# Performance work log

Hardware: AMD Instinct MI355X
Metric: run time of the kernel (lower is better)

Reference implementation:

```python
import jax, jax.numpy as jnp
import numpy as np

N = 50000      # num nodes (genes)
E = 800000     # num edges (TF->Target)
IN = 128       # in_channels
HID = 16       # hidden_channels per head
HEADS = 4
OUT = 32       # out_channels
NEG_SLOPE = 0.2  # PyG GATConv leaky_relu slope
EPS = 1e-16


def setup_inputs() -> dict:
    key = jax.random.key(0)
    ks = jax.random.split(key, 11)
    x = jax.random.normal(ks[0], (N, IN), dtype=jnp.float32)
    edge_index = jax.random.randint(ks[1], (2, E), 0, N, dtype=jnp.int32)
    # layer 1: heads=HEADS, concat=True
    W1 = jax.random.normal(ks[2], (IN, HEADS * HID), dtype=jnp.float32) * (1.0 / np.sqrt(IN))
    a_src1 = jax.random.normal(ks[3], (HEADS, HID), dtype=jnp.float32) * 0.1
    a_dst1 = jax.random.normal(ks[4], (HEADS, HID), dtype=jnp.float32) * 0.1
    b1 = jnp.zeros((HEADS * HID,), dtype=jnp.float32)
    # layer 2: heads=1, concat=False
    W2 = jax.random.normal(ks[5], (HEADS * HID, OUT), dtype=jnp.float32) * (1.0 / np.sqrt(HEADS * HID))
    a_src2 = jax.random.normal(ks[6], (1, OUT), dtype=jnp.float32) * 0.1
    a_dst2 = jax.random.normal(ks[7], (1, OUT), dtype=jnp.float32) * 0.1
    b2 = jnp.zeros((OUT,), dtype=jnp.float32)
    return dict(x=x, edge_index=edge_index, W1=W1, a_src1=a_src1, a_dst1=a_dst1, b1=b1,
                W2=W2, a_src2=a_src2, a_dst2=a_dst2, b2=b2)


def gat_layer(x, edge_index, W, a_src, a_dst, b, concat):
    """PyG GATConv (no self-loops, eval mode): gather -> edge attention -> segment softmax -> scatter."""
    n = x.shape[0]
    heads, ch = a_src.shape
    h = (x @ W).reshape(n, heads, ch)                      # [N, H, C]
    alpha_s = jnp.einsum('nhc,hc->nh', h, a_src)           # [N, H]
    alpha_d = jnp.einsum('nhc,hc->nh', h, a_dst)           # [N, H]
    src, dst = edge_index[0], edge_index[1]
    e = jax.nn.leaky_relu(alpha_s[src] + alpha_d[dst], negative_slope=NEG_SLOPE)  # [E, H]
    # numerically stable softmax over incoming edges of each dst node
    m = jax.ops.segment_max(e, dst, num_segments=n)        # [N, H]
    e = jnp.exp(e - m[dst])
    denom = jax.ops.segment_sum(e, dst, num_segments=n)    # [N, H]
    alpha = e / (denom[dst] + EPS)                         # [E, H]
    msg = h[src] * alpha[:, :, None]                       # [E, H, C]
    out = jax.ops.segment_sum(msg, dst, num_segments=n)    # [N, H, C]
    if concat:
        out = out.reshape(n, heads * ch)
    else:
        out = out.mean(axis=1)
    return out + b


def reference(x, edge_index, W1, a_src1, a_dst1, b1, W2, a_src2, a_dst2, b2):
    h = gat_layer(x, edge_index, W1, a_src1, a_dst1, b1, concat=True)   # [N, HEADS*HID]
    h = jax.nn.elu(h)
    out = gat_layer(h, edge_index, W2, a_src2, a_dst2, b2, concat=False)  # [N, OUT]
    return out
```

## Files before the change

kernel.cpp:

```cpp
#include <hip/hip_runtime.h>
#include <math.h>

#define NN 50000
#define NE 800000
#define INCH 128
#define HID1 16
#define H1 4
#define C1 64
#define C2 32
#define NEG 0.2f
#define EPSF 1e-16f
#define CAP 128
#define BSH 7
#define NBKT 391
#define CAPB 3072
#define EPB 2048
#define NPB1 391

static __device__ __forceinline__ float lrelu(float v){ return v > 0.f ? v : NEG * v; }


__global__ __launch_bounds__(256) void k_part1(const int* __restrict__ ei, int* bcnt,
                                               int2* __restrict__ pairs){
    __shared__ int hist[512];
    __shared__ int scn[512];
    __shared__ int spos[512];
    __shared__ int gbase[NBKT];
    __shared__ int2 stg[EPB];
    int t = threadIdx.x;
    hist[t] = 0; hist[t + 256] = 0;
    __syncthreads();

    int e0 = blockIdx.x * EPB;
    int tot = NE - e0; if (tot > EPB) tot = EPB;
    int srcv[8], dstv[8], rnk[8], bkt[8];
    #pragma unroll
    for (int k = 0; k < 8; ++k){
        int idx = k * 256 + t;
        if (idx < tot){
            int e = e0 + idx;
            srcv[k] = ei[e];
            dstv[k] = ei[NE + e];
            bkt[k] = dstv[k] >> BSH;
            rnk[k] = atomicAdd(&hist[bkt[k]], 1);
        } else bkt[k] = -1;
    }
    __syncthreads();

    int* sA = hist; int* sB = scn;
    for (int off = 1; off < 512; off <<= 1){
        int v0 = sA[t]       + ((t       >= off) ? sA[t - off]       : 0);
        int v1 = sA[t + 256] + ((t + 256 >= off) ? sA[t + 256 - off] : 0);
        __syncthreads();
        sB[t] = v0; sB[t + 256] = v1;
        __syncthreads();
        int* tmp = sA; sA = sB; sB = tmp;
    }
    for (int b = t; b < NBKT; b += 256){
        int incl = sA[b];
        int excl = (b > 0) ? sA[b - 1] : 0;
        spos[b] = excl;
        int cnt = incl - excl;
        gbase[b] = (cnt > 0) ? atomicAdd(&bcnt[b], cnt) : 0;
    }
    __syncthreads();

    #pragma unroll
    for (int k = 0; k < 8; ++k)
        if (bkt[k] >= 0){
            int2 pr; pr.x = srcv[k]; pr.y = dstv[k];
            stg[spos[bkt[k]] + rnk[k]] = pr;
        }
    __syncthreads();

    for (int i = t; i < tot; i += 256){
        int2 pr = stg[i];
        int b = pr.y >> BSH;
        pairs[(size_t)b * CAPB + gbase[b] + (i - spos[b])] = pr;
    }
}

__global__ __launch_bounds__(256) void k_part2(const int2* __restrict__ pairs,
                                               const int* __restrict__ bcnt,
                                               int* __restrict__ rows, int* __restrict__ deg,
                                               int* __restrict__ srcs){
    __shared__ int2 stg[CAPB];
    __shared__ int hist[128], scn[128], cur[128];
    int b = blockIdx.x, t = threadIdx.x;
    int n0 = b << BSH;
    int cnt = bcnt[b];
    if (t < 128) hist[t] = 0;
    __syncthreads();
    const int2* psrc = pairs + (size_t)b * CAPB;
    for (int i = t; i < cnt; i += 256){
        int2 pr = psrc[i];
        stg[i] = pr;
        atomicAdd(&hist[pr.y - n0], 1);
    }
    __syncthreads();
    int v = (t < 128) ? hist[t] : 0;
    if (t < 128) scn[t] = v;
    __syncthreads();
    for (int off = 1; off < 128; off <<= 1){
        int add = (t < 128 && t >= off) ? scn[t - off] : 0;
        __syncthreads();
        if (t < 128) scn[t] += add;
        __syncthreads();
    }
    if (t < 128){
        int base = b * CAPB + (scn[t] - v);
        cur[t] = base;
        int n = n0 + t;
        if (n < NN){ rows[n] = base; deg[n] = v; }
    }
    __syncthreads();
    for (int i = t; i < cnt; i += 256){
        int2 pr = stg[i];
        int p = atomicAdd(&cur[pr.y - n0], 1);
        srcs[p] = pr.x;
    }
}


__global__ void k_gemm1(const float* __restrict__ x, const float* __restrict__ W,
                        const float* __restrict__ asrc, const float* __restrict__ adst,
                        float* __restrict__ h, float* __restrict__ as1, float* __restrict__ ad1){
    __shared__ float XT[INCH][68];
    __shared__ float WS[INCH * C1];
    __shared__ float ps[64][17];
    __shared__ float pd[64][17];

    int t = threadIdx.x;
    int nodeL = t >> 2;
    int kc = t & 3;
    int g = blockIdx.x * 64 + nodeL;
    int gc = min(g, NN - 1);
    const float4* xr = (const float4*)(x + (size_t)gc * INCH);
    #pragma unroll
    for (int i = 0; i < 8; ++i){
        int k = kc * 32 + i * 4;
        float4 v = xr[k >> 2];
        XT[k + 0][nodeL] = v.x;
        XT[k + 1][nodeL] = v.y;
        XT[k + 2][nodeL] = v.z;
        XT[k + 3][nodeL] = v.w;
    }
    const float4* W4 = (const float4*)W;
    float4* WS4 = (float4*)WS;
    #pragma unroll
    for (int i = 0; i < 8; ++i) WS4[i * 256 + t] = W4[i * 256 + t];
    __syncthreads();

    int tx = t & 15, ty = t >> 4;
    int c4 = tx * 4, n4 = ty * 4;
    float acc[4][4];
    #pragma unroll
    for (int a = 0; a < 4; ++a)
        #pragma unroll
        for (int b = 0; b < 4; ++b) acc[a][b] = 0.f;

    #pragma unroll 8
    for (int k = 0; k < INCH; ++k){
        float4 xa = *(const float4*)&XT[k][n4];
        float4 wb = *(const float4*)&WS[k * C1 + c4];
        const float xv[4] = {xa.x, xa.y, xa.z, xa.w};
        const float wv[4] = {wb.x, wb.y, wb.z, wb.w};
        #pragma unroll
        for (int a = 0; a < 4; ++a)
            #pragma unroll
            for (int b = 0; b < 4; ++b)
                acc[a][b] = fmaf(xv[a], wv[b], acc[a][b]);
    }

    int hd = tx >> 2;
    #pragma unroll
    for (int a = 0; a < 4; ++a){
        int n = blockIdx.x * 64 + n4 + a;
        if (n < NN){
            float4 o = {acc[a][0], acc[a][1], acc[a][2], acc[a][3]};
            *(float4*)&h[(size_t)n * C1 + c4] = o;
        }
        float sa = 0.f, da = 0.f;
        #pragma unroll
        for (int b = 0; b < 4; ++b){
            float wsv = asrc[hd * HID1 + (c4 & 15) + b];
            float wdv = adst[hd * HID1 + (c4 & 15) + b];
            sa = fmaf(acc[a][b], wsv, sa);
            da = fmaf(acc[a][b], wdv, da);
        }
        ps[n4 + a][tx] = sa;
        pd[n4 + a][tx] = da;
    }
    __syncthreads();
    int nd = t & 63, hh = t >> 6;
    int g2 = blockIdx.x * 64 + nd;
    if (g2 < NN){
        float sa = ps[nd][hh*4+0] + ps[nd][hh*4+1] + ps[nd][hh*4+2] + ps[nd][hh*4+3];
        float da = pd[nd][hh*4+0] + pd[nd][hh*4+1] + pd[nd][hh*4+2] + pd[nd][hh*4+3];
        as1[g2 * H1 + hh] = sa;
        ad1[g2 * H1 + hh] = da;
    }
}


__global__ void k_gemm2(const float* __restrict__ hp, const float* __restrict__ W2,
                        const float* __restrict__ asrc, const float* __restrict__ adst,
                        float* __restrict__ h2, float* __restrict__ as2, float* __restrict__ ad2){
    __shared__ float XT[C1][132];
    __shared__ float WS[C1 * C2];
    __shared__ float ps[128][9];
    __shared__ float pd[128][9];

    int t = threadIdx.x;
    int nodeL = t >> 1;
    int kc = t & 1;
    int g = blockIdx.x * 128 + nodeL;
    int gc = min(g, NN - 1);
    const float4* xr = (const float4*)(hp + (size_t)gc * C1);
    #pragma unroll
    for (int i = 0; i < 8; ++i){
        int k = kc * 32 + i * 4;
        float4 v = xr[k >> 2];
        XT[k + 0][nodeL] = v.x;
        XT[k + 1][nodeL] = v.y;
        XT[k + 2][nodeL] = v.z;
        XT[k + 3][nodeL] = v.w;
    }
    const float4* W4 = (const float4*)W2;
    float4* WS4 = (float4*)WS;
    #pragma unroll
    for (int i = 0; i < 2; ++i) WS4[i * 256 + t] = W4[i * 256 + t];
    __syncthreads();

    int tx = t & 7, ty = t >> 3;
    int c4 = tx * 4, n4 = ty * 4;
    float acc[4][4];
    #pragma unroll
    for (int a = 0; a < 4; ++a)
        #pragma unroll
        for (int b = 0; b < 4; ++b) acc[a][b] = 0.f;

    #pragma unroll 8
    for (int k = 0; k < C1; ++k){
        float4 xa = *(const float4*)&XT[k][n4];
        float4 wb = *(const float4*)&WS[k * C2 + c4];
        const float xv[4] = {xa.x, xa.y, xa.z, xa.w};
        const float wv[4] = {wb.x, wb.y, wb.z, wb.w};
        #pragma unroll
        for (int a = 0; a < 4; ++a)
            #pragma unroll
            for (int b = 0; b < 4; ++b)
                acc[a][b] = fmaf(xv[a], wv[b], acc[a][b]);
    }

    #pragma unroll
    for (int a = 0; a < 4; ++a){
        int n = blockIdx.x * 128 + n4 + a;
        if (n < NN){
            float4 o = {acc[a][0], acc[a][1], acc[a][2], acc[a][3]};
            *(float4*)&h2[(size_t)n * C2 + c4] = o;
        }
        float sa = 0.f, da = 0.f;
        #pragma unroll
        for (int b = 0; b < 4; ++b){
            sa = fmaf(acc[a][b], asrc[c4 + b], sa);
            da = fmaf(acc[a][b], adst[c4 + b], da);
        }
        ps[n4 + a][tx] = sa;
        pd[n4 + a][tx] = da;
    }
    __syncthreads();
    if (t < 128){
        int n = blockIdx.x * 128 + t;
        if (n < NN){
            float sa = 0.f, da = 0.f;
            #pragma unroll
            for (int i = 0; i < 8; ++i){ sa += ps[t][i]; da += pd[t][i]; }
            as2[n] = sa;
            ad2[n] = da;
        }
    }
}


__global__ __launch_bounds__(256) void k_agg1(
        const int* __restrict__ srcs, const int* __restrict__ rows,
        const int* __restrict__ deg, const float* __restrict__ h,
        const float* __restrict__ as, const float* __restrict__ ad,
        const float* __restrict__ b1, float* __restrict__ hp){
    __shared__ float vbuf[4][CAP * H1];
    __shared__ int   sbuf[4][CAP];
    __shared__ float minv[4][8];
    int wv = threadIdx.x >> 6;
    int lane = threadIdx.x & 63;
    int node = blockIdx.x * 4 + wv;
    int hd = lane >> 4, sub = lane & 15;
    int start = rows[node], dg = deg[node];
    float adv = ad[node * H1 + hd];
    bool fits = (dg <= CAP);

    float m = -1e30f, ssum = 0.f;
    for (int j = sub; j < dg; j += 16){
        int s = srcs[start + j];
        float v = lrelu(as[s * H1 + hd] + adv);
        if (fits){
            vbuf[wv][j * H1 + hd] = v;
            if (hd == 0) sbuf[wv][j] = s;
        }
        float nm = fmaxf(m, v);
        ssum = ssum * __expf(m - nm) + __expf(v - nm);
        m = nm;
    }
    #pragma unroll
    for (int off = 1; off < 16; off <<= 1){
        float om = __shfl_xor(m, off);
        float os = __shfl_xor(ssum, off);
        float nm = fmaxf(m, om);
        ssum = ssum * __expf(m - nm) + os * __expf(om - nm);
        m = nm;
    }
    float inv = 1.f / (ssum + EPSF);
    if (sub == 0){ minv[wv][hd] = m; minv[wv][4 + hd] = inv; }
    __syncthreads();

    if (fits){
        int tot = dg * H1;
        for (int it = lane; it < tot; it += 64){
            int th = it & 3;
            vbuf[wv][it] = __expf(vbuf[wv][it] - minv[wv][th]) * minv[wv][4 + th];
        }
    }
    __syncthreads();

    float acc0 = 0.f, acc1 = 0.f;
    const float* hL = h + lane;
    if (fits){
        int j = 0;
        for (; j + 3 < dg; j += 4){
            int s0 = sbuf[wv][j], s1 = sbuf[wv][j+1], s2 = sbuf[wv][j+2], s3 = sbuf[wv][j+3];
            float w0 = vbuf[wv][(j+0)*H1+hd], w1 = vbuf[wv][(j+1)*H1+hd];
            float w2 = vbuf[wv][(j+2)*H1+hd], w3 = vbuf[wv][(j+3)*H1+hd];
            float g0 = hL[(size_t)s0 * C1], g1 = hL[(size_t)s1 * C1];
            float g2 = hL[(size_t)s2 * C1], g3 = hL[(size_t)s3 * C1];
            acc0 = fmaf(g0, w0, acc0);
            acc1 = fmaf(g1, w1, acc1);
            acc0 = fmaf(g2, w2, acc0);
            acc1 = fmaf(g3, w3, acc1);
        }
        for (; j < dg; ++j)
            acc0 = fmaf(hL[(size_t)sbuf[wv][j] * C1], vbuf[wv][j*H1+hd], acc0);
    } else {
        for (int j = 0; j < dg; ++j){
            int s = srcs[start + j];
            float v = lrelu(as[s * H1 + hd] + adv);
            acc0 = fmaf(hL[(size_t)s * C1], __expf(v - m) * inv, acc0);
        }
    }
    float o = acc0 + acc1 + b1[lane];
    hp[(size_t)node * C1 + lane] = o > 0.f ? o : expm1f(o);
}

__global__ __launch_bounds__(256) void k_agg2(
        const int* __restrict__ srcs, const int* __restrict__ rows,
        const int* __restrict__ deg, const float* __restrict__ h2,
        const float* __restrict__ as, const float* __restrict__ ad,
        const float* __restrict__ b2, float* __restrict__ out){
    __shared__ float vbuf[8][CAP];
    __shared__ int   sbuf[8][CAP];
    int sl = threadIdx.x >> 5;
    int lane = threadIdx.x & 31;
    int node = blockIdx.x * 8 + sl;
    int start = rows[node], dg = deg[node];
    float adv = ad[node];
    bool fits = (dg <= CAP);

    float m = -1e30f, ssum = 0.f;
    for (int j = lane; j < dg; j += 32){
        int s = srcs[start + j];
        float v = lrelu(as[s] + adv);
        if (fits){ vbuf[sl][j] = v; sbuf[sl][j] = s; }
        float nm = fmaxf(m, v);
        ssum = ssum * __expf(m - nm) + __expf(v - nm);
        m = nm;
    }
    #pragma unroll
    for (int off = 1; off < 32; off <<= 1){
        float om = __shfl_xor(m, off);
        float os = __shfl_xor(ssum, off);
        float nm = fmaxf(m, om);
        ssum = ssum * __expf(m - nm) + os * __expf(om - nm);
        m = nm;
    }
    float inv = 1.f / (ssum + EPSF);
    if (fits)
        for (int j = lane; j < dg; j += 32)
            vbuf[sl][j] = __expf(vbuf[sl][j] - m) * inv;
    __syncthreads();

    float acc0 = 0.f, acc1 = 0.f;
    const float* hL = h2 + lane;
    if (fits){
        int j = 0;
        for (; j + 3 < dg; j += 4){
            int s0 = sbuf[sl][j], s1 = sbuf[sl][j+1], s2 = sbuf[sl][j+2], s3 = sbuf[sl][j+3];
            float w0 = vbuf[sl][j], w1 = vbuf[sl][j+1], w2 = vbuf[sl][j+2], w3 = vbuf[sl][j+3];
            float g0 = hL[(size_t)s0 * C2], g1 = hL[(size_t)s1 * C2];
            float g2 = hL[(size_t)s2 * C2], g3 = hL[(size_t)s3 * C2];
            acc0 = fmaf(g0, w0, acc0);
            acc1 = fmaf(g1, w1, acc1);
            acc0 = fmaf(g2, w2, acc0);
            acc1 = fmaf(g3, w3, acc1);
        }
        for (; j < dg; ++j)
            acc0 = fmaf(hL[(size_t)sbuf[sl][j] * C2], vbuf[sl][j], acc0);
    } else {
        for (int j = 0; j < dg; ++j){
            int s = srcs[start + j];
            acc0 = fmaf(hL[(size_t)s * C2], __expf(lrelu(as[s] + adv) - m) * inv, acc0);
        }
    }
    out[(size_t)node * C2 + lane] = acc0 + acc1 + b2[lane];
}

extern "C" void kernel_launch(void* const* d_in, const int* in_sizes, int n_in,
                              void* d_out, int out_size, void* d_ws, size_t ws_size,
                              hipStream_t stream) {
    const float* x    = (const float*)d_in[0];
    const int*   ei   = (const int*)  d_in[1];
    const float* W1   = (const float*)d_in[2];
    const float* as1w = (const float*)d_in[3];
    const float* ad1w = (const float*)d_in[4];
    const float* b1   = (const float*)d_in[5];
    const float* W2   = (const float*)d_in[6];
    const float* as2w = (const float*)d_in[7];
    const float* ad2w = (const float*)d_in[8];
    const float* b2   = (const float*)d_in[9];
    float* out = (float*)d_out;

    float* p = (float*)d_ws;
    float* h1   = p; p += (size_t)NN * C1;
    float* hp   = p; p += (size_t)NN * C1;
    float* as1  = p; p += (size_t)NN * H1;
    float* ad1  = p; p += (size_t)NN * H1;
    float* h2   = p; p += (size_t)NN * C2;
    float* as2  = p; p += NN;
    float* ad2  = p; p += NN;
    int* deg  = (int*)p; p += NN;
    int* rows = (int*)p; p += NN;
    int* bcnt = (int*)p; p += NBKT;
    int* srcs = (int*)p; p += (size_t)NBKT * CAPB;
    int2* pairs = (int2*)h1;

    dim3 B(256);
    hipMemsetAsync(bcnt, 0, NBKT * sizeof(int), stream);
    k_part1 <<<NPB1, B, 0, stream>>>(ei, bcnt, pairs);
    k_part2 <<<NBKT, B, 0, stream>>>(pairs, bcnt, rows, deg, srcs);
    k_gemm1 <<<(NN + 63) / 64, B, 0, stream>>>(x, W1, as1w, ad1w, h1, as1, ad1);
    k_agg1  <<<NN / 4, B, 0, stream>>>(srcs, rows, deg, h1, as1, ad1, b1, hp);
    k_gemm2 <<<(NN + 127) / 128, B, 0, stream>>>(hp, W2, as2w, ad2w, h2, as2, ad2);
    k_agg2  <<<NN / 8, B, 0, stream>>>(srcs, rows, deg, h2, as2, ad2, b2, out);
}
```

Before: 205.1 us.

## Fuse CSR build with GEMM1, fuse agg1 with GEMM2, drop softmax max pass

The CSR bucket build and the layer-1 GEMM now run as one launch, with blocks split by blockIdx, so both can overlap. Layer-1 aggregation is fused with the layer-2 GEMM and attention projection, so the hp intermediate is never written or read back. Both aggregation kernels drop the max-subtracted two-pass softmax in favour of a single pass that sums unnormalized exp weights and divides once at the end. That removes the shared-memory staging and a second pass over the edges, but exp can overflow if attention logits grow large.

```diff
diff --git a/kernel.cpp b/kernel.cpp
--- a/kernel.cpp
+++ b/kernel.cpp
@@ -10,12 +10,12 @@
 #define C2 32
 #define NEG 0.2f
 #define EPSF 1e-16f
-#define CAP 128
 #define BSH 7
 #define NBKT 391
 #define CAPB 3072
 #define EPB 2048
 #define NPB1 391
+#define GB1 782
 
 static __device__ __forceinline__ float lrelu(float v){ return v > 0.f ? v : NEG * v; }
 
@@ -80,346 +80,237 @@
     }
 }
 
-__global__ __launch_bounds__(256) void k_part2(const int2* __restrict__ pairs,
-                                               const int* __restrict__ bcnt,
-                                               int* __restrict__ rows, int* __restrict__ deg,
-                                               int* __restrict__ srcs){
-    __shared__ int2 stg[CAPB];
-    __shared__ int hist[128], scn[128], cur[128];
-    int b = blockIdx.x, t = threadIdx.x;
-    int n0 = b << BSH;
-    int cnt = bcnt[b];
-    if (t < 128) hist[t] = 0;
-    __syncthreads();
-    const int2* psrc = pairs + (size_t)b * CAPB;
-    for (int i = t; i < cnt; i += 256){
-        int2 pr = psrc[i];
-        stg[i] = pr;
-        atomicAdd(&hist[pr.y - n0], 1);
-    }
-    __syncthreads();
-    int v = (t < 128) ? hist[t] : 0;
-    if (t < 128) scn[t] = v;
-    __syncthreads();
-    for (int off = 1; off < 128; off <<= 1){
-        int add = (t < 128 && t >= off) ? scn[t - off] : 0;
-        __syncthreads();
-        if (t < 128) scn[t] += add;
-        __syncthreads();
-    }
-    if (t < 128){
-        int base = b * CAPB + (scn[t] - v);
-        cur[t] = base;
-        int n = n0 + t;
-        if (n < NN){ rows[n] = base; deg[n] = v; }
-    }
-    __syncthreads();
-    for (int i = t; i < cnt; i += 256){
-        int2 pr = stg[i];
-        int p = atomicAdd(&cur[pr.y - n0], 1);
-        srcs[p] = pr.x;
-    }
-}
-
-
-__global__ void k_gemm1(const float* __restrict__ x, const float* __restrict__ W,
-                        const float* __restrict__ asrc, const float* __restrict__ adst,
-                        float* __restrict__ h, float* __restrict__ as1, float* __restrict__ ad1){
-    __shared__ float XT[INCH][68];
-    __shared__ float WS[INCH * C1];
-    __shared__ float ps[64][17];
-    __shared__ float pd[64][17];
-
+
+__global__ __launch_bounds__(256) void k_build2(
+        const int2* __restrict__ pairs, const int* __restrict__ bcnt,
+        int* __restrict__ rows, int* __restrict__ deg, int* __restrict__ srcs,
+        const float* __restrict__ x, const float* __restrict__ W,
+        const float* __restrict__ asrc, const float* __restrict__ adst,
+        float* __restrict__ h, float* __restrict__ as1, float* __restrict__ ad1){
+    __shared__ __align__(16) char smem[76288];
     int t = threadIdx.x;
-    int nodeL = t >> 2;
-    int kc = t & 3;
-    int g = blockIdx.x * 64 + nodeL;
-    int gc = min(g, NN - 1);
-    const float4* xr = (const float4*)(x + (size_t)gc * INCH);
-    #pragma unroll
-    for (int i = 0; i < 8; ++i){
-        int k = kc * 32 + i * 4;
-        float4 v = xr[k >> 2];
-        XT[k + 0][nodeL] = v.x;
-        XT[k + 1][nodeL] = v.y;
-        XT[k + 2][nodeL] = v.z;
-        XT[k + 3][nodeL] = v.w;
-    }
-    const float4* W4 = (const float4*)W;
-    float4* WS4 = (float4*)WS;
-    #pragma unroll
-    for (int i = 0; i < 8; ++i) WS4[i * 256 + t] = W4[i * 256 + t];
-    __syncthreads();
-
-    int tx = t & 15, ty = t >> 4;
-    int c4 = tx * 4, n4 = ty * 4;
-    float acc[4][4];
-    #pragma unroll
-    for (int a = 0; a < 4; ++a)
+
+    if (blockIdx.x < NBKT){
+        int2* stg = (int2*)smem;
+        int* hist = (int*)(smem + 24576);
+        int* scn  = (int*)(smem + 25088);
+        int* cur  = (int*)(smem + 25600);
+        int b = blockIdx.x;
+        int n0 = b << BSH;
+        int cnt = bcnt[b];
+        if (t < 128) hist[t] = 0;
+        __syncthreads();
+        const int2* psrc = pairs + (size_t)b * CAPB;
+        for (int i = t; i < cnt; i += 256){
+            int2 pr = psrc[i];
+            stg[i] = pr;
+            atomicAdd(&hist[pr.y - n0], 1);
+        }
+        __syncthreads();
+        int v = (t < 128) ? hist[t] : 0;
+        if (t < 128) scn[t] = v;
+        __syncthreads();
+        for (int off = 1; off < 128; off <<= 1){
+            int add = (t < 128 && t >= off) ? scn[t - off] : 0;
+            __syncthreads();
+            if (t < 128) scn[t] += add;
+            __syncthreads();
+        }
+        if (t < 128){
+            int base = b * CAPB + (scn[t] - v);
+            cur[t] = base;
+            int n = n0 + t;
+            if (n < NN){ rows[n] = base; deg[n] = v; }
+        }
+        __syncthreads();
+        for (int i = t; i < cnt; i += 256){
+            int2 pr = stg[i];
+            int p = atomicAdd(&cur[pr.y - n0], 1);
+            srcs[p] = pr.x;
+        }
+    } else {
+        float (*XT)[68] = (float(*)[68])smem;
+        float* WS = (float*)(smem + 34816);
+        float (*ps)[17] = (float(*)[17])(smem + 67584);
+        float (*pd)[17] = (float(*)[17])(smem + 71936);
+        int bid = blockIdx.x - NBKT;
+
+        int nodeL = t >> 2;
+        int kc = t & 3;
+        int g = bid * 64 + nodeL;
+        int gc = min(g, NN - 1);
+        const float4* xr = (const float4*)(x + (size_t)gc * INCH);
         #pragma unroll
-        for (int b = 0; b < 4; ++b) acc[a][b] = 0.f;
-
-    #pragma unroll 8
-    for (int k = 0; k < INCH; ++k){
-        float4 xa = *(const float4*)&XT[k][n4];
-        float4 wb = *(const float4*)&WS[k * C1 + c4];
-        const float xv[4] = {xa.x, xa.y, xa.z, xa.w};
-        const float wv[4] = {wb.x, wb.y, wb.z, wb.w};
+        for (int i = 0; i < 8; ++i){
+            int k = kc * 32 + i * 4;
+            float4 v = xr[k >> 2];
+            XT[k + 0][nodeL] = v.x;
+            XT[k + 1][nodeL] = v.y;
+            XT[k + 2][nodeL] = v.z;
+            XT[k + 3][nodeL] = v.w;
+        }
+        const float4* W4 = (const float4*)W;
+        float4* WS4 = (float4*)WS;
+        #pragma unroll
+        for (int i = 0; i < 8; ++i) WS4[i * 256 + t] = W4[i * 256 + t];
+        __syncthreads();
+
+        int tx = t & 15, ty = t >> 4;
+        int c4 = tx * 4, n4 = ty * 4;
+        float acc[4][4];
         #pragma unroll
         for (int a = 0; a < 4; ++a)
             #pragma unroll
-            for (int b = 0; b < 4; ++b)
-                acc[a][b] = fmaf(xv[a], wv[b], acc[a][b]);
-    }
-
-    int hd = tx >> 2;
+            for (int b2 = 0; b2 < 4; ++b2) acc[a][b2] = 0.f;
+
+        #pragma unroll 8
+        for (int k = 0; k < INCH; ++k){
+            float4 xa = *(const float4*)&XT[k][n4];
+            float4 wb = *(const float4*)&WS[k * C1 + c4];
+            const float xv[4] = {xa.x, xa.y, xa.z, xa.w};
+            const float wv[4] = {wb.x, wb.y, wb.z, wb.w};
+            #pragma unroll
+            for (int a = 0; a < 4; ++a)
+                #pragma unroll
+                for (int b2 = 0; b2 < 4; ++b2)
+                    acc[a][b2] = fmaf(xv[a], wv[b2], acc[a][b2]);
+        }
+
+        int hd = tx >> 2;
+        #pragma unroll
+        for (int a = 0; a < 4; ++a){
+            int n = bid * 64 + n4 + a;
+            if (n < NN){
+                float4 o = {acc[a][0], acc[a][1], acc[a][2], acc[a][3]};
+                *(float4*)&h[(size_t)n * C1 + c4] = o;
+            }
+            float sa = 0.f, da = 0.f;
+            #pragma unroll
+            for (int b2 = 0; b2 < 4; ++b2){
+                sa = fmaf(acc[a][b2], asrc[hd * HID1 + (c4 & 15) + b2], sa);
+                da = fmaf(acc[a][b2], adst[hd * HID1 + (c4 & 15) + b2], da);
+            }
+            ps[n4 + a][tx] = sa;
+            pd[n4 + a][tx] = da;
+        }
+        __syncthreads();
+        int nd = t & 63, hh = t >> 6;
+        int g2 = bid * 64 + nd;
+        if (g2 < NN){
+            float sa = ps[nd][hh*4+0] + ps[nd][hh*4+1] + ps[nd][hh*4+2] + ps[nd][hh*4+3];
+            float da = pd[nd][hh*4+0] + pd[nd][hh*4+1] + pd[nd][hh*4+2] + pd[nd][hh*4+3];
+            as1[g2 * H1 + hh] = sa;
+            ad1[g2 * H1 + hh] = da;
+        }
+    }
+}
+
+
+__global__ __launch_bounds__(256) void k_aggA(
+        const int* __restrict__ srcs, const int* __restrict__ rows,
+        const int* __restrict__ deg, const float* __restrict__ h1,
+        const float* __restrict__ as, const float* __restrict__ ad,
+        const float* __restrict__ b1, const float* __restrict__ W2,
+        const float* __restrict__ a2s, const float* __restrict__ a2d,
+        float* __restrict__ h2, float* __restrict__ as2, float* __restrict__ ad2){
+    __shared__ float hpT[16][65];
+    __shared__ float WS[C1 * C2];
+    int t = threadIdx.x;
+    {
+        const float4* W4 = (const float4*)W2;
+        float4* WS4 = (float4*)WS;
+        WS4[t] = W4[t];
+        WS4[256 + t] = W4[256 + t];
+    }
+    int w = t >> 6, lane = t & 63, hd = lane >> 4;
+    float bv = b1[lane];
     #pragma unroll
-    for (int a = 0; a < 4; ++a){
-        int n = blockIdx.x * 64 + n4 + a;
-        if (n < NN){
-            float4 o = {acc[a][0], acc[a][1], acc[a][2], acc[a][3]};
-            *(float4*)&h[(size_t)n * C1 + c4] = o;
-        }
-        float sa = 0.f, da = 0.f;
-        #pragma unroll
-        for (int b = 0; b < 4; ++b){
-            float wsv = asrc[hd * HID1 + (c4 & 15) + b];
-            float wdv = adst[hd * HID1 + (c4 & 15) + b];
-            sa = fmaf(acc[a][b], wsv, sa);
-            da = fmaf(acc[a][b], wdv, da);
-        }
-        ps[n4 + a][tx] = sa;
-        pd[n4 + a][tx] = da;
-    }
-    __syncthreads();
-    int nd = t & 63, hh = t >> 6;
-    int g2 = blockIdx.x * 64 + nd;
-    if (g2 < NN){
-        float sa = ps[nd][hh*4+0] + ps[nd][hh*4+1] + ps[nd][hh*4+2] + ps[nd][hh*4+3];
-        float da = pd[nd][hh*4+0] + pd[nd][hh*4+1] + pd[nd][hh*4+2] + pd[nd][hh*4+3];
-        as1[g2 * H1 + hh] = sa;
-        ad1[g2 * H1 + hh] = da;
-    }
-}
-
-
-__global__ void k_gemm2(const float* __restrict__ hp, const float* __restrict__ W2,
-                        const float* __restrict__ asrc, const float* __restrict__ adst,
-                        float* __restrict__ h2, float* __restrict__ as2, float* __restrict__ ad2){
-    __shared__ float XT[C1][132];
-    __shared__ float WS[C1 * C2];
-    __shared__ float ps[128][9];
-    __shared__ float pd[128][9];
-
-    int t = threadIdx.x;
-    int nodeL = t >> 1;
-    int kc = t & 1;
-    int g = blockIdx.x * 128 + nodeL;
-    int gc = min(g, NN - 1);
-    const float4* xr = (const float4*)(hp + (size_t)gc * C1);
-    #pragma unroll
-    for (int i = 0; i < 8; ++i){
-        int k = kc * 32 + i * 4;
-        float4 v = xr[k >> 2];
-        XT[k + 0][nodeL] = v.x;
-        XT[k + 1][nodeL] = v.y;
-        XT[k + 2][nodeL] = v.z;
-        XT[k + 3][nodeL] = v.w;
-    }
-    const float4* W4 = (const float4*)W2;
-    float4* WS4 = (float4*)WS;
-    #pragma unroll
-    for (int i = 0; i < 2; ++i) WS4[i * 256 + t] = W4[i * 256 + t];
-    __syncthreads();
-
-    int tx = t & 7, ty = t >> 3;
-    int c4 = tx * 4, n4 = ty * 4;
-    float acc[4][4];
-    #pragma unroll
-    for (int a = 0; a < 4; ++a)
-        #pragma unroll
-        for (int b = 0; b < 4; ++b) acc[a][b] = 0.f;
-
+    for (int q = 0; q < 4; ++q){
+        int node = blockIdx.x * 16 + w * 4 + q;
+        int start = rows[node], dg = deg[node];
+        float adv = ad[node * H1 + hd];
+        const float* hL = h1 + lane;
+        float ss0 = 0.f, ss1 = 0.f, ac0 = 0.f, ac1 = 0.f, ac2 = 0.f, ac3 = 0.f;
+        int j = 0;
+        for (; j + 3 < dg; j += 4){
+            int s0 = srcs[start + j], s1 = srcs[start + j + 1];
+            int s2 = srcs[start + j + 2], s3 = srcs[start + j + 3];
+            float w0 = __expf(lrelu(as[s0 * H1 + hd] + adv));
+            float w1 = __expf(lrelu(as[s1 * H1 + hd] + adv));
+            float w2 = __expf(lrelu(as[s2 * H1 + hd] + adv));
+            float w3 = __expf(lrelu(as[s3 * H1 + hd] + adv));
+            ss0 += w0 + w2; ss1 += w1 + w3;
+            ac0 = fmaf(hL[(size_t)s0 * C1], w0, ac0);
+            ac1 = fmaf(hL[(size_t)s1 * C1], w1, ac1);
+            ac2 = fmaf(hL[(size_t)s2 * C1], w2, ac2);
+            ac3 = fmaf(hL[(size_t)s3 * C1], w3, ac3);
+        }
+        for (; j < dg; ++j){
+            int s = srcs[start + j];
+            float wv = __expf(lrelu(as[s * H1 + hd] + adv));
+            ss0 += wv;
+            ac0 = fmaf(hL[(size_t)s * C1], wv, ac0);
+        }
+        float o = (ac0 + ac1 + ac2 + ac3) / (ss0 + ss1 + EPSF) + bv;
+        hpT[w * 4 + q][lane] = o > 0.f ? o : expm1f(o);
+    }
+    __syncthreads();
+
+    int n = t >> 4, c = t & 15;
+    float a0 = 0.f, a1 = 0.f;
     #pragma unroll 8
     for (int k = 0; k < C1; ++k){
-        float4 xa = *(const float4*)&XT[k][n4];
-        float4 wb = *(const float4*)&WS[k * C2 + c4];
-        const float xv[4] = {xa.x, xa.y, xa.z, xa.w};
-        const float wv[4] = {wb.x, wb.y, wb.z, wb.w};
-        #pragma unroll
-        for (int a = 0; a < 4; ++a)
-            #pragma unroll
-            for (int b = 0; b < 4; ++b)
-                acc[a][b] = fmaf(xv[a], wv[b], acc[a][b]);
-    }
-
+        float hv = hpT[n][k];
+        a0 = fmaf(hv, WS[k * C2 + c], a0);
+        a1 = fmaf(hv, WS[k * C2 + c + 16], a1);
+    }
+    int gn = blockIdx.x * 16 + n;
+    h2[(size_t)gn * C2 + c] = a0;
+    h2[(size_t)gn * C2 + c + 16] = a1;
+    float sa = a0 * a2s[c] + a1 * a2s[c + 16];
+    float da = a0 * a2d[c] + a1 * a2d[c + 16];
     #pragma unroll
-    for (int a = 0; a < 4; ++a){
-        int n = blockIdx.x * 128 + n4 + a;
-        if (n < NN){
-            float4 o = {acc[a][0], acc[a][1], acc[a][2], acc[a][3]};
-            *(float4*)&h2[(size_t)n * C2 + c4] = o;
-        }
-        float sa = 0.f, da = 0.f;
-        #pragma unroll
-        for (int b = 0; b < 4; ++b){
-            sa = fmaf(acc[a][b], asrc[c4 + b], sa);
-            da = fmaf(acc[a][b], adst[c4 + b], da);
-        }
-        ps[n4 + a][tx] = sa;
-        pd[n4 + a][tx] = da;
-    }
-    __syncthreads();
-    if (t < 128){
-        int n = blockIdx.x * 128 + t;
-        if (n < NN){
-            float sa = 0.f, da = 0.f;
-            #pragma unroll
-            for (int i = 0; i < 8; ++i){ sa += ps[t][i]; da += pd[t][i]; }
-            as2[n] = sa;
-            ad2[n] = da;
-        }
-    }
-}
-
-
-__global__ __launch_bounds__(256) void k_agg1(
-        const int* __restrict__ srcs, const int* __restrict__ rows,
-        const int* __restrict__ deg, const float* __restrict__ h,
-        const float* __restrict__ as, const float* __restrict__ ad,
-        const float* __restrict__ b1, float* __restrict__ hp){
-    __shared__ float vbuf[4][CAP * H1];
-    __shared__ int   sbuf[4][CAP];
-    __shared__ float minv[4][8];
-    int wv = threadIdx.x >> 6;
-    int lane = threadIdx.x & 63;
-    int node = blockIdx.x * 4 + wv;
-    int hd = lane >> 4, sub = lane & 15;
-    int start = rows[node], dg = deg[node];
-    float adv = ad[node * H1 + hd];
-    bool fits = (dg <= CAP);
-
-    float m = -1e30f, ssum = 0.f;
-    for (int j = sub; j < dg; j += 16){
-        int s = srcs[start + j];
-        float v = lrelu(as[s * H1 + hd] + adv);
-        if (fits){
-            vbuf[wv][j * H1 + hd] = v;
-            if (hd == 0) sbuf[wv][j] = s;
-        }
-        float nm = fmaxf(m, v);
-        ssum = ssum * __expf(m - nm) + __expf(v - nm);
-        m = nm;
-    }
-    #pragma unroll
-    for (int off = 1; off < 16; off <<= 1){
-        float om = __shfl_xor(m, off);
-        float os = __shfl_xor(ssum, off);
-        float nm = fmaxf(m, om);
-        ssum = ssum * __expf(m - nm) + os * __expf(om - nm);
-        m = nm;
-    }
-    float inv = 1.f / (ssum + EPSF);
-    if (sub == 0){ minv[wv][hd] = m; minv[wv][4 + hd] = inv; }
-    __syncthreads();
-
-    if (fits){
-        int tot = dg * H1;
-        for (int it = lane; it < tot; it += 64){
-            int th = it & 3;
-            vbuf[wv][it] = __expf(vbuf[wv][it] - minv[wv][th]) * minv[wv][4 + th];
-        }
-    }
-    __syncthreads();
-
-    float acc0 = 0.f, acc1 = 0.f;
-    const float* hL = h + lane;
-    if (fits){
-        int j = 0;
-        for (; j + 3 < dg; j += 4){
-            int s0 = sbuf[wv][j], s1 = sbuf[wv][j+1], s2 = sbuf[wv][j+2], s3 = sbuf[wv][j+3];
-            float w0 = vbuf[wv][(j+0)*H1+hd], w1 = vbuf[wv][(j+1)*H1+hd];
-            float w2 = vbuf[wv][(j+2)*H1+hd], w3 = vbuf[wv][(j+3)*H1+hd];
-            float g0 = hL[(size_t)s0 * C1], g1 = hL[(size_t)s1 * C1];
-            float g2 = hL[(size_t)s2 * C1], g3 = hL[(size_t)s3 * C1];
-            acc0 = fmaf(g0, w0, acc0);
-            acc1 = fmaf(g1, w1, acc1);
-            acc0 = fmaf(g2, w2, acc0);
-            acc1 = fmaf(g3, w3, acc1);
-        }
-        for (; j < dg; ++j)
-            acc0 = fmaf(hL[(size_t)sbuf[wv][j] * C1], vbuf[wv][j*H1+hd], acc0);
-    } else {
-        for (int j = 0; j < dg; ++j){
-            int s = srcs[start + j];
-            float v = lrelu(as[s * H1 + hd] + adv);
-            acc0 = fmaf(hL[(size_t)s * C1], __expf(v - m) * inv, acc0);
-        }
-    }
-    float o = acc0 + acc1 + b1[lane];
-    hp[(size_t)node * C1 + lane] = o > 0.f ? o : expm1f(o);
-}
+    for (int off = 8; off >= 1; off >>= 1){
+        sa += __shfl_xor(sa, off);
+        da += __shfl_xor(da, off);
+    }
+    if (c == 0){ as2[gn] = sa; ad2[gn] = da; }
+}
+
 
 __global__ __launch_bounds__(256) void k_agg2(
         const int* __restrict__ srcs, const int* __restrict__ rows,
         const int* __restrict__ deg, const float* __restrict__ h2,
         const float* __restrict__ as, const float* __restrict__ ad,
         const float* __restrict__ b2, float* __restrict__ out){
-    __shared__ float vbuf[8][CAP];
-    __shared__ int   sbuf[8][CAP];
     int sl = threadIdx.x >> 5;
     int lane = threadIdx.x & 31;
     int node = blockIdx.x * 8 + sl;
     int start = rows[node], dg = deg[node];
     float adv = ad[node];
-    bool fits = (dg <= CAP);
-
-    float m = -1e30f, ssum = 0.f;
-    for (int j = lane; j < dg; j += 32){
+    const float* hL = h2 + lane;
+    float ss0 = 0.f, ss1 = 0.f, ac0 = 0.f, ac1 = 0.f, ac2 = 0.f, ac3 = 0.f;
+    int j = 0;
+    for (; j + 3 < dg; j += 4){
+        int s0 = srcs[start + j], s1 = srcs[start + j + 1];
+        int s2 = srcs[start + j + 2], s3 = srcs[start + j + 3];
+        float w0 = __expf(lrelu(as[s0] + adv));
+        float w1 = __expf(lrelu(as[s1] + adv));
+        float w2 = __expf(lrelu(as[s2] + adv));
+        float w3 = __expf(lrelu(as[s3] + adv));
+        ss0 += w0 + w2; ss1 += w1 + w3;
+        ac0 = fmaf(hL[(size_t)s0 * C2], w0, ac0);
+        ac1 = fmaf(hL[(size_t)s1 * C2], w1, ac1);
+        ac2 = fmaf(hL[(size_t)s2 * C2], w2, ac2);
+        ac3 = fmaf(hL[(size_t)s3 * C2], w3, ac3);
+    }
+    for (; j < dg; ++j){
         int s = srcs[start + j];
-        float v = lrelu(as[s] + adv);
-        if (fits){ vbuf[sl][j] = v; sbuf[sl][j] = s; }
-        float nm = fmaxf(m, v);
-        ssum = ssum * __expf(m - nm) + __expf(v - nm);
-        m = nm;
-    }
-    #pragma unroll
-    for (int off = 1; off < 32; off <<= 1){
-        float om = __shfl_xor(m, off);
-        float os = __shfl_xor(ssum, off);
-        float nm = fmaxf(m, om);
-        ssum = ssum * __expf(m - nm) + os * __expf(om - nm);
-        m = nm;
-    }
-    float inv = 1.f / (ssum + EPSF);
-    if (fits)
-        for (int j = lane; j < dg; j += 32)
-            vbuf[sl][j] = __expf(vbuf[sl][j] - m) * inv;
-    __syncthreads();
-
-    float acc0 = 0.f, acc1 = 0.f;
-    const float* hL = h2 + lane;
-    if (fits){
-        int j = 0;
-        for (; j + 3 < dg; j += 4){
-            int s0 = sbuf[sl][j], s1 = sbuf[sl][j+1], s2 = sbuf[sl][j+2], s3 = sbuf[sl][j+3];
-            float w0 = vbuf[sl][j], w1 = vbuf[sl][j+1], w2 = vbuf[sl][j+2], w3 = vbuf[sl][j+3];
-            float g0 = hL[(size_t)s0 * C2], g1 = hL[(size_t)s1 * C2];
-            float g2 = hL[(size_t)s2 * C2], g3 = hL[(size_t)s3 * C2];
-            acc0 = fmaf(g0, w0, acc0);
-            acc1 = fmaf(g1, w1, acc1);
-            acc0 = fmaf(g2, w2, acc0);
-            acc1 = fmaf(g3, w3, acc1);
-        }
-        for (; j < dg; ++j)
-            acc0 = fmaf(hL[(size_t)sbuf[sl][j] * C2], vbuf[sl][j], acc0);
-    } else {
-        for (int j = 0; j < dg; ++j){
-            int s = srcs[start + j];
-            acc0 = fmaf(hL[(size_t)s * C2], __expf(lrelu(as[s] + adv) - m) * inv, acc0);
-        }
-    }
-    out[(size_t)node * C2 + lane] = acc0 + acc1 + b2[lane];
+        float wv = __expf(lrelu(as[s] + adv));
+        ss0 += wv;
+        ac0 = fmaf(hL[(size_t)s * C2], wv, ac0);
+    }
+    out[(size_t)node * C2 + lane] = (ac0 + ac1 + ac2 + ac3) / (ss0 + ss1 + EPSF) + b2[lane];
 }
 
 extern "C" void kernel_launch(void* const* d_in, const int* in_sizes, int n_in,
@@ -439,7 +330,6 @@
 
     float* p = (float*)d_ws;
     float* h1   = p; p += (size_t)NN * C1;
-    float* hp   = p; p += (size_t)NN * C1;
     float* as1  = p; p += (size_t)NN * H1;
     float* ad1  = p; p += (size_t)NN * H1;
     float* h2   = p; p += (size_t)NN * C2;
@@ -447,16 +337,16 @@
     float* ad2  = p; p += NN;
     int* deg  = (int*)p; p += NN;
     int* rows = (int*)p; p += NN;
-    int* bcnt = (int*)p; p += NBKT;
+    int* bcnt = (int*)p; p += NBKT + 57;
     int* srcs = (int*)p; p += (size_t)NBKT * CAPB;
-    int2* pairs = (int2*)h1;
+    int2* pairs = (int2*)p;
 
     dim3 B(256);
     hipMemsetAsync(bcnt, 0, NBKT * sizeof(int), stream);
     k_part1 <<<NPB1, B, 0, stream>>>(ei, bcnt, pairs);
-    k_part2 <<<NBKT, B, 0, stream>>>(pairs, bcnt, rows, deg, srcs);
-    k_gemm1 <<<(NN + 63) / 64, B, 0, stream>>>(x, W1, as1w, ad1w, h1, as1, ad1);
-    k_agg1  <<<NN / 4, B, 0, stream>>>(srcs, rows, deg, h1, as1, ad1, b1, hp);
-    k_gemm2 <<<(NN + 127) / 128, B, 0, stream>>>(hp, W2, as2w, ad2w, h2, as2, ad2);
+    k_build2<<<NBKT + GB1, B, 0, stream>>>(pairs, bcnt, rows, deg, srcs,
+                                           x, W1, as1w, ad1w, h1, as1, ad1);
+    k_aggA  <<<NN / 16, B, 0, stream>>>(srcs, rows, deg, h1, as1, ad1, b1,
+                                        W2, as2w, ad2w, h2, as2, ad2);
     k_agg2  <<<NN / 8, B, 0, stream>>>(srcs, rows, deg, h2, as2, ad2, b2, out);
 }
```

Measured after the change: 197.5 us. -3.7%, faster.
